# Optimization experiments

Measured on AMD Instinct MI355X. Metric: run time of the kernel, lower is better.

## Reference

```python
import jax, jax.numpy as jnp
import numpy as np

N = 12000
E = 384000
F_IN, F_HID, F_OUT = 512, 256, 64


def setup_inputs() -> dict:
    key = jax.random.key(0)
    ks = jax.random.split(key, 8)
    x = jax.random.normal(ks[0], (N, F_IN), dtype=jnp.float32)
    edge_index = jax.random.randint(ks[1], (2, E), 0, N, dtype=jnp.int64)
    s = lambda fi: 1.0 / np.sqrt(fi)  # glorot-ish scaling
    W1 = jax.random.normal(ks[2], (F_IN, F_HID), dtype=jnp.float32) * s(F_IN)
    W2 = jax.random.normal(ks[3], (F_HID, F_HID), dtype=jnp.float32) * s(F_HID)
    Wmu = jax.random.normal(ks[4], (F_HID, F_OUT), dtype=jnp.float32) * s(F_HID)
    Wls = jax.random.normal(ks[5], (F_HID, F_OUT), dtype=jnp.float32) * s(F_HID)
    return {
        "x": x, "edge_index": edge_index,
        "W1": W1, "b1": jnp.zeros((F_HID,), jnp.float32),
        "W2": W2, "b2": jnp.zeros((F_HID,), jnp.float32),
        "Wmu": Wmu, "bmu": jnp.zeros((F_OUT,), jnp.float32),
        "Wls": Wls, "bls": jnp.zeros((F_OUT,), jnp.float32),
    }


def _gcn_norm(edge_index, n):
    # add self-loops, symmetric normalization D^-1/2 (A+I) D^-1/2 (PyG gcn_norm)
    loop = jnp.arange(n, dtype=edge_index.dtype)
    row = jnp.concatenate([edge_index[0], loop])
    col = jnp.concatenate([edge_index[1], loop])
    deg = jax.ops.segment_sum(jnp.ones(row.shape[0], jnp.float32), col, num_segments=n)
    dinv = jnp.where(deg > 0, jax.lax.rsqrt(jnp.maximum(deg, 1.0)), 0.0)
    norm = dinv[row] * dinv[col]  # [E + n]
    return row, col, norm


def _gcn_conv(h, W, b, row, col, norm, n):
    hw = h @ W                                    # [n, f_out] linear first
    msg = norm[:, None] * hw[row]                 # gather + per-edge scale
    out = jax.ops.segment_sum(msg, col, num_segments=n)  # scatter-add
    return out + b


def reference(x, edge_index, W1, b1, W2, b2, Wmu, bmu, Wls, bls):
    n = x.shape[0]
    row, col, norm = _gcn_norm(edge_index, n)
    h = jax.nn.relu(_gcn_conv(x, W1, b1, row, col, norm, n))
    h = jax.nn.relu(_gcn_conv(h, W2, b2, row, col, norm, n))
    mu = _gcn_conv(h, Wmu, bmu, row, col, norm, n)
    logstd = _gcn_conv(h, Wls, bls, row, col, norm, n)  # computed by encode; unused in eval z
    z = mu  # VGAE.reparametrize in eval mode returns mu (deterministic reference)
    adj_pred = jax.nn.sigmoid(z @ z.T)  # InnerProductDecoder.forward_all
    return adj_pred
```

## Files before the change

kernel.cpp:

```cpp
#include <hip/hip_runtime.h>

#define NN   12000
#define NE   384000
#define FIN  512
#define FHID 256
#define FOUT 64

typedef unsigned short u16;
typedef __attribute__((ext_vector_type(8))) short  s8v;
typedef __attribute__((ext_vector_type(4))) float  f4v;

__device__ __forceinline__ u16 f2bf(float f) {
    union { float f; unsigned int i; } v; v.f = f;
    return (u16)((v.i + 0x7FFFu + ((v.i >> 16) & 1u)) >> 16);
}


__global__ void k_deg(const int* __restrict__ col, float* __restrict__ deg) {
    int e = blockIdx.x * 256 + threadIdx.x;
    if (e < NE) atomicAdd(&deg[col[e]], 1.0f);
}

__global__ __launch_bounds__(1024) void k_scan(const float* __restrict__ deg,
                                               float* __restrict__ dinv,
                                               int* __restrict__ offs,
                                               int* __restrict__ cursor) {
    __shared__ int sh[1024];
    int tid = threadIdx.x;
    int base = tid * 12;
    int loc[12];
    int sum = 0;
    for (int j = 0; j < 12; j++) {
        int i = base + j;
        int d = (i < NN) ? (int)deg[i] : 0;
        loc[j] = sum;
        sum += d;
    }
    sh[tid] = sum;
    __syncthreads();
    for (int off = 1; off < 1024; off <<= 1) {
        int v = (tid >= off) ? sh[tid - off] : 0;
        __syncthreads();
        sh[tid] += v;
        __syncthreads();
    }
    int prev = (tid == 0) ? 0 : sh[tid - 1];
    for (int j = 0; j < 12; j++) {
        int i = base + j;
        if (i < NN) {
            int o = prev + loc[j];
            offs[i] = o;
            cursor[i] = o;
            dinv[i] = rsqrtf(deg[i] + 1.0f);
        }
    }
    if (tid == 0) offs[NN] = NE;
}

__global__ void k_fill(const int* __restrict__ row, const int* __restrict__ col,
                       int* __restrict__ cursor, int* __restrict__ csr) {
    int e = blockIdx.x * 256 + threadIdx.x;
    if (e < NE) {
        int c = col[e];
        int p = atomicAdd(&cursor[c], 1);
        csr[p] = row[e];
    }
}

__global__ void k_repack(const float* __restrict__ B, u16* __restrict__ Bp, int K, int N) {
    int idx = blockIdx.x * 256 + threadIdx.x;
    int total = (N >> 4) * (K >> 5) * 64;
    if (idx >= total) return;
    int l  = idx & 63;
    int ts = idx >> 6;
    int Ks = K >> 5;
    int s  = ts % Ks;
    int t  = ts / Ks;
    int q = l >> 4, r = l & 15;
    s8v v;
    #pragma unroll
    for (int j = 0; j < 8; j++)
        v[j] = (short)f2bf(B[(s * 32 + q * 8 + j) * N + t * 16 + r]);
    ((s8v*)Bp)[idx] = v;
}

template <int K, int N>
__global__ __launch_bounds__(256) void k_gemm(const float* __restrict__ A,
                                              const u16* __restrict__ Bp,
                                              const float* __restrict__ dinv,
                                              float* __restrict__ C) {
    constexpr int KS = K / 32;
    int wave = threadIdx.x >> 6, lane = threadIdx.x & 63;
    int q = lane >> 4, r = lane & 15;
    int row0 = blockIdx.x * 64 + wave * 16;
    if (row0 >= NN) return;
    int tb = blockIdx.y * 4;

    f4v acc[4];
    #pragma unroll
    for (int t = 0; t < 4; t++) acc[t] = (f4v){0.f, 0.f, 0.f, 0.f};

    const float* arow = A + (size_t)(row0 + r) * K + q * 8;
    #pragma unroll 4
    for (int s = 0; s < KS; s++) {
        f4v f0 = *(const f4v*)(arow + s * 32);
        f4v f1 = *(const f4v*)(arow + s * 32 + 4);
        s8v a;
        #pragma unroll
        for (int j = 0; j < 4; j++) { a[j] = (short)f2bf(f0[j]); a[4 + j] = (short)f2bf(f1[j]); }
        #pragma unroll
        for (int t = 0; t < 4; t++) {
            s8v b = *(const s8v*)(Bp + ((((size_t)(tb + t) * KS + s) * 64 + lane) << 3));
            acc[t] = __builtin_amdgcn_mfma_f32_16x16x32_bf16(a, b, acc[t], 0, 0, 0);
        }
    }
    float dv[4];
    #pragma unroll
    for (int rr = 0; rr < 4; rr++) dv[rr] = dinv[row0 + q * 4 + rr];
    #pragma unroll
    for (int t = 0; t < 4; t++) {
        int n = (tb + t) * 16 + r;
        #pragma unroll
        for (int rr = 0; rr < 4; rr++) {
            int m = row0 + q * 4 + rr;
            C[(size_t)m * N + n] = acc[t][rr] * dv[rr];
        }
    }
}

template <int FPL, bool RELU>
__global__ __launch_bounds__(256) void k_agg(const float* __restrict__ hw,
                                             const int* __restrict__ csr,
                                             const int* __restrict__ offs,
                                             const float* __restrict__ dinv,
                                             const float* __restrict__ bias,
                                             float* __restrict__ out) {
    constexpr int F = FPL * 64;
    int wg = (blockIdx.x * 256 + threadIdx.x) >> 6;
    if (wg >= NN) return;
    int lane = threadIdx.x & 63;
    int c = wg;

    float acc[FPL];
    {
        const float* p = hw + (size_t)c * F + lane * FPL;
        if constexpr (FPL == 4) {
            f4v v = *(const f4v*)p;
            #pragma unroll
            for (int k = 0; k < 4; k++) acc[k] = v[k];
        } else {
            acc[0] = *p;
        }
    }
    int beg = offs[c], end = offs[c + 1];
    for (int e = beg; e < end; e += 64) {
        int nb = end - e; if (nb > 64) nb = 64;
        int myid = (e + lane < end) ? csr[e + lane] : 0;
        for (int j = 0; j < nb; j++) {
            int src = __shfl(myid, j, 64);
            const float* p = hw + (size_t)src * F + lane * FPL;
            if constexpr (FPL == 4) {
                f4v v = *(const f4v*)p;
                #pragma unroll
                for (int k = 0; k < 4; k++) acc[k] += v[k];
            } else {
                acc[0] += *p;
            }
        }
    }
    float dv = dinv[c];
    if constexpr (FPL == 4) {
        f4v ov;
        #pragma unroll
        for (int k = 0; k < 4; k++) {
            float val = acc[k] * dv + bias[lane * 4 + k];
            if (RELU) val = fmaxf(val, 0.f);
            ov[k] = val;
        }
        *(f4v*)(out + (size_t)c * F + lane * 4) = ov;
    } else {
        float val = acc[0] * dv + bias[lane];
        if (RELU) val = fmaxf(val, 0.f);
        out[(size_t)c * F + lane] = val;
    }
}

__global__ __launch_bounds__(256) void k_dec(const float* __restrict__ mu, float* __restrict__ out) {
    int wave = threadIdx.x >> 6, lane = threadIdx.x & 63;
    int q = lane >> 4, r = lane & 15;
    int row0 = blockIdx.y * 64 + wave * 16;
    if (row0 >= NN) return;
    int col0 = blockIdx.x * 64;

    s8v a0, a1;
    {
        const float* ap = mu + (size_t)(row0 + r) * FOUT + q * 8;
        f4v f0 = *(const f4v*)(ap);
        f4v f1 = *(const f4v*)(ap + 4);
        f4v f2 = *(const f4v*)(ap + 32);
        f4v f3 = *(const f4v*)(ap + 36);
        #pragma unroll
        for (int j = 0; j < 4; j++) {
            a0[j] = (short)f2bf(f0[j]); a0[4 + j] = (short)f2bf(f1[j]);
            a1[j] = (short)f2bf(f2[j]); a1[4 + j] = (short)f2bf(f3[j]);
        }
    }

    #pragma unroll
    for (int t = 0; t < 4; t++) {
        int n0 = col0 + t * 16;
        if (n0 >= NN) return;
        s8v b0, b1;
        const float* bp = mu + (size_t)(n0 + r) * FOUT + q * 8;
        f4v f0 = *(const f4v*)(bp);
        f4v f1 = *(const f4v*)(bp + 4);
        f4v f2 = *(const f4v*)(bp + 32);
        f4v f3 = *(const f4v*)(bp + 36);
        #pragma unroll
        for (int j = 0; j < 4; j++) {
            b0[j] = (short)f2bf(f0[j]); b0[4 + j] = (short)f2bf(f1[j]);
            b1[j] = (short)f2bf(f2[j]); b1[4 + j] = (short)f2bf(f3[j]);
        }
        f4v acc = (f4v){0.f, 0.f, 0.f, 0.f};
        acc = __builtin_amdgcn_mfma_f32_16x16x32_bf16(a0, b0, acc, 0, 0, 0);
        acc = __builtin_amdgcn_mfma_f32_16x16x32_bf16(a1, b1, acc, 0, 0, 0);
        #pragma unroll
        for (int rr = 0; rr < 4; rr++) {
            int m = row0 + q * 4 + rr;
            float sg = 1.0f / (1.0f + __expf(-acc[rr]));
            out[(size_t)m * NN + (n0 + r)] = sg;
        }
    }
}

extern "C" void kernel_launch(void* const* d_in, const int* in_sizes, int n_in,
                              void* d_out, int out_size, void* d_ws, size_t ws_size,
                              hipStream_t stream) {
    const float* x   = (const float*)d_in[0];
    const int*   ei  = (const int*)d_in[1];
    const float* W1  = (const float*)d_in[2];
    const float* b1  = (const float*)d_in[3];
    const float* W2  = (const float*)d_in[4];
    const float* b2  = (const float*)d_in[5];
    const float* Wmu = (const float*)d_in[6];
    const float* bmu = (const float*)d_in[7];

    char* w = (char*)d_ws;
    size_t off = 0;
    auto alloc = [&](size_t bytes) {
        void* p = w + off;
        off = (off + bytes + 255) & ~(size_t)255;
        return p;
    };
    float* deg    = (float*)alloc(NN * 4);
    float* dinv   = (float*)alloc(NN * 4);
    int*   offs   = (int*)alloc((NN + 1) * 4);
    int*   cursor = (int*)alloc(NN * 4);
    int*   csr    = (int*)alloc(NE * 4);
    float* hw     = (float*)alloc((size_t)NN * FHID * 4);
    float* hA     = (float*)alloc((size_t)NN * FHID * 4);
    float* hB     = (float*)alloc((size_t)NN * FHID * 4);
    float* muB    = (float*)alloc((size_t)NN * FOUT * 4);
    u16*   W1p    = (u16*)alloc((size_t)FIN * FHID * 2);
    u16*   W2p    = (u16*)alloc((size_t)FHID * FHID * 2);
    u16*   Wmp    = (u16*)alloc((size_t)FHID * FOUT * 2);

    const int* erow = ei;
    const int* ecol = ei + NE;

    hipMemsetAsync(deg, 0, NN * 4, stream);
    k_deg<<<(NE + 255) / 256, 256, 0, stream>>>(ecol, deg);
    k_scan<<<1, 1024, 0, stream>>>(deg, dinv, offs, cursor);
    k_fill<<<(NE + 255) / 256, 256, 0, stream>>>(erow, ecol, cursor, csr);

    k_repack<<<((FIN / 32) * (FHID / 16) * 64 + 255) / 256, 256, 0, stream>>>(W1, W1p, FIN, FHID);
    k_repack<<<((FHID / 32) * (FHID / 16) * 64 + 255) / 256, 256, 0, stream>>>(W2, W2p, FHID, FHID);
    k_repack<<<((FHID / 32) * (FOUT / 16) * 64 + 255) / 256, 256, 0, stream>>>(Wmu, Wmp, FHID, FOUT);

    dim3 blk(256);
    k_gemm<FIN, FHID><<<dim3(188, FHID / 64), blk, 0, stream>>>(x, W1p, dinv, hw);
    k_agg<4, true><<<NN / 4, blk, 0, stream>>>(hw, csr, offs, dinv, b1, hA);
    k_gemm<FHID, FHID><<<dim3(188, FHID / 64), blk, 0, stream>>>(hA, W2p, dinv, hw);
    k_agg<4, true><<<NN / 4, blk, 0, stream>>>(hw, csr, offs, dinv, b2, hB);
    k_gemm<FHID, FOUT><<<dim3(188, FOUT / 64), blk, 0, stream>>>(hB, Wmp, dinv, hw);
    k_agg<1, false><<<NN / 4, blk, 0, stream>>>(hw, csr, offs, dinv, bmu, muB);
    k_dec<<<dim3(188, 188), blk, 0, stream>>>(muB, (float*)d_out);
}
```

Baseline: 1.051 ms.

## Vectorize output stores via swapped MFMA operands, bf16 mu, unrolled gathers

Result: faster. 907.4 us (-13.7%).

```diff
diff --git a/kernel.cpp b/kernel.cpp
--- a/kernel.cpp
+++ b/kernel.cpp
@@ -111,125 +111,130 @@
         #pragma unroll
         for (int t = 0; t < 4; t++) {
             s8v b = *(const s8v*)(Bp + ((((size_t)(tb + t) * KS + s) * 64 + lane) << 3));
-            acc[t] = __builtin_amdgcn_mfma_f32_16x16x32_bf16(a, b, acc[t], 0, 0, 0);
-        }
-    }
-    float dv[4];
-    #pragma unroll
-    for (int rr = 0; rr < 4; rr++) dv[rr] = dinv[row0 + q * 4 + rr];
+            acc[t] = __builtin_amdgcn_mfma_f32_16x16x32_bf16(b, a, acc[t], 0, 0, 0);
+        }
+    }
+    float dv = dinv[row0 + r];
+    float* crow = C + (size_t)(row0 + r) * N;
     #pragma unroll
     for (int t = 0; t < 4; t++) {
-        int n = (tb + t) * 16 + r;
-        #pragma unroll
-        for (int rr = 0; rr < 4; rr++) {
-            int m = row0 + q * 4 + rr;
-            C[(size_t)m * N + n] = acc[t][rr] * dv[rr];
-        }
-    }
-}
-
-template <int FPL, bool RELU>
+        f4v ov = acc[t] * dv;
+        *(f4v*)(crow + (tb + t) * 16 + q * 4) = ov;
+    }
+}
+
+template <bool RELU>
 __global__ __launch_bounds__(256) void k_agg(const float* __restrict__ hw,
                                              const int* __restrict__ csr,
                                              const int* __restrict__ offs,
                                              const float* __restrict__ dinv,
                                              const float* __restrict__ bias,
                                              float* __restrict__ out) {
-    constexpr int F = FPL * 64;
+    constexpr int F = 256;
     int wg = (blockIdx.x * 256 + threadIdx.x) >> 6;
     if (wg >= NN) return;
     int lane = threadIdx.x & 63;
     int c = wg;
-
-    float acc[FPL];
-    {
-        const float* p = hw + (size_t)c * F + lane * FPL;
-        if constexpr (FPL == 4) {
-            f4v v = *(const f4v*)p;
-            #pragma unroll
-            for (int k = 0; k < 4; k++) acc[k] = v[k];
-        } else {
-            acc[0] = *p;
-        }
-    }
+    const float* hp = hw + lane * 4;
+
+    f4v acc = *(const f4v*)(hp + (size_t)c * F);
     int beg = offs[c], end = offs[c + 1];
     for (int e = beg; e < end; e += 64) {
         int nb = end - e; if (nb > 64) nb = 64;
         int myid = (e + lane < end) ? csr[e + lane] : 0;
-        for (int j = 0; j < nb; j++) {
-            int src = __shfl(myid, j, 64);
-            const float* p = hw + (size_t)src * F + lane * FPL;
-            if constexpr (FPL == 4) {
-                f4v v = *(const f4v*)p;
-                #pragma unroll
-                for (int k = 0; k < 4; k++) acc[k] += v[k];
-            } else {
-                acc[0] += *p;
-            }
+        int j = 0;
+        for (; j + 4 <= nb; j += 4) {
+            int s0 = __shfl(myid, j, 64);
+            int s1 = __shfl(myid, j + 1, 64);
+            int s2 = __shfl(myid, j + 2, 64);
+            int s3 = __shfl(myid, j + 3, 64);
+            f4v v0 = *(const f4v*)(hp + (size_t)s0 * F);
+            f4v v1 = *(const f4v*)(hp + (size_t)s1 * F);
+            f4v v2 = *(const f4v*)(hp + (size_t)s2 * F);
+            f4v v3 = *(const f4v*)(hp + (size_t)s3 * F);
+            v0 += v1; v2 += v3;
+            acc += v0 + v2;
+        }
+        for (; j < nb; j++) {
+            int s0 = __shfl(myid, j, 64);
+            acc += *(const f4v*)(hp + (size_t)s0 * F);
         }
     }
     float dv = dinv[c];
-    if constexpr (FPL == 4) {
-        f4v ov;
-        #pragma unroll
-        for (int k = 0; k < 4; k++) {
-            float val = acc[k] * dv + bias[lane * 4 + k];
-            if (RELU) val = fmaxf(val, 0.f);
-            ov[k] = val;
-        }
-        *(f4v*)(out + (size_t)c * F + lane * 4) = ov;
-    } else {
-        float val = acc[0] * dv + bias[lane];
-        if (RELU) val = fmaxf(val, 0.f);
-        out[(size_t)c * F + lane] = val;
-    }
-}
-
-__global__ __launch_bounds__(256) void k_dec(const float* __restrict__ mu, float* __restrict__ out) {
+    f4v bv = *(const f4v*)(bias + lane * 4);
+    f4v ov = acc * dv + bv;
+    if (RELU) {
+        #pragma unroll
+        for (int k = 0; k < 4; k++) ov[k] = fmaxf(ov[k], 0.f);
+    }
+    *(f4v*)(out + (size_t)c * F + lane * 4) = ov;
+}
+
+__global__ __launch_bounds__(256) void k_agg_mu(const float* __restrict__ hw,
+                                                const int* __restrict__ csr,
+                                                const int* __restrict__ offs,
+                                                const float* __restrict__ dinv,
+                                                const float* __restrict__ bias,
+                                                u16* __restrict__ out) {
+    constexpr int F = 64;
+    int wg = (blockIdx.x * 256 + threadIdx.x) >> 6;
+    if (wg >= NN) return;
+    int lane = threadIdx.x & 63;
+    int c = wg;
+    const float* hp = hw + lane;
+
+    float acc = hp[(size_t)c * F];
+    int beg = offs[c], end = offs[c + 1];
+    for (int e = beg; e < end; e += 64) {
+        int nb = end - e; if (nb > 64) nb = 64;
+        int myid = (e + lane < end) ? csr[e + lane] : 0;
+        int j = 0;
+        for (; j + 4 <= nb; j += 4) {
+            int s0 = __shfl(myid, j, 64);
+            int s1 = __shfl(myid, j + 1, 64);
+            int s2 = __shfl(myid, j + 2, 64);
+            int s3 = __shfl(myid, j + 3, 64);
+            float v0 = hp[(size_t)s0 * F];
+            float v1 = hp[(size_t)s1 * F];
+            float v2 = hp[(size_t)s2 * F];
+            float v3 = hp[(size_t)s3 * F];
+            acc += (v0 + v1) + (v2 + v3);
+        }
+        for (; j < nb; j++)
+            acc += hp[(size_t)__shfl(myid, j, 64) * F];
+    }
+    out[(size_t)c * F + lane] = f2bf(acc * dinv[c] + bias[lane]);
+}
+
+__global__ __launch_bounds__(256) void k_dec(const u16* __restrict__ mu, float* __restrict__ out) {
     int wave = threadIdx.x >> 6, lane = threadIdx.x & 63;
     int q = lane >> 4, r = lane & 15;
     int row0 = blockIdx.y * 64 + wave * 16;
     if (row0 >= NN) return;
     int col0 = blockIdx.x * 64;
 
-    s8v a0, a1;
-    {
-        const float* ap = mu + (size_t)(row0 + r) * FOUT + q * 8;
-        f4v f0 = *(const f4v*)(ap);
-        f4v f1 = *(const f4v*)(ap + 4);
-        f4v f2 = *(const f4v*)(ap + 32);
-        f4v f3 = *(const f4v*)(ap + 36);
-        #pragma unroll
-        for (int j = 0; j < 4; j++) {
-            a0[j] = (short)f2bf(f0[j]); a0[4 + j] = (short)f2bf(f1[j]);
-            a1[j] = (short)f2bf(f2[j]); a1[4 + j] = (short)f2bf(f3[j]);
-        }
-    }
+    const u16* ap = mu + (size_t)(row0 + r) * FOUT + q * 8;
+    s8v a0 = *(const s8v*)(ap);
+    s8v a1 = *(const s8v*)(ap + 32);
+    float* orow = out + (size_t)(row0 + r) * NN;
 
     #pragma unroll
     for (int t = 0; t < 4; t++) {
         int n0 = col0 + t * 16;
         if (n0 >= NN) return;
-        s8v b0, b1;
-        const float* bp = mu + (size_t)(n0 + r) * FOUT + q * 8;
-        f4v f0 = *(const f4v*)(bp);
-        f4v f1 = *(const f4v*)(bp + 4);
-        f4v f2 = *(const f4v*)(bp + 32);
-        f4v f3 = *(const f4v*)(bp + 36);
-        #pragma unroll
-        for (int j = 0; j < 4; j++) {
-            b0[j] = (short)f2bf(f0[j]); b0[4 + j] = (short)f2bf(f1[j]);
-            b1[j] = (short)f2bf(f2[j]); b1[4 + j] = (short)f2bf(f3[j]);
-        }
+        const u16* bp = mu + (size_t)(n0 + r) * FOUT + q * 8;
+        s8v b0 = *(const s8v*)(bp);
+        s8v b1 = *(const s8v*)(bp + 32);
         f4v acc = (f4v){0.f, 0.f, 0.f, 0.f};
-        acc = __builtin_amdgcn_mfma_f32_16x16x32_bf16(a0, b0, acc, 0, 0, 0);
-        acc = __builtin_amdgcn_mfma_f32_16x16x32_bf16(a1, b1, acc, 0, 0, 0);
+        acc = __builtin_amdgcn_mfma_f32_16x16x32_bf16(b0, a0, acc, 0, 0, 0);
+        acc = __builtin_amdgcn_mfma_f32_16x16x32_bf16(b1, a1, acc, 0, 0, 0);
+        f4v ov;
         #pragma unroll
         for (int rr = 0; rr < 4; rr++) {
-            int m = row0 + q * 4 + rr;
-            float sg = 1.0f / (1.0f + __expf(-acc[rr]));
-            out[(size_t)m * NN + (n0 + r)] = sg;
-        }
+            float e = __expf(-acc[rr]);
+            ov[rr] = __builtin_amdgcn_rcpf(1.0f + e);
+        }
+        *(f4v*)(orow + n0 + q * 4) = ov;
     }
 }
 
@@ -260,7 +265,7 @@
     float* hw     = (float*)alloc((size_t)NN * FHID * 4);
     float* hA     = (float*)alloc((size_t)NN * FHID * 4);
     float* hB     = (float*)alloc((size_t)NN * FHID * 4);
-    float* muB    = (float*)alloc((size_t)NN * FOUT * 4);
+    u16*   muB    = (u16*)alloc((size_t)NN * FOUT * 2);
     u16*   W1p    = (u16*)alloc((size_t)FIN * FHID * 2);
     u16*   W2p    = (u16*)alloc((size_t)FHID * FHID * 2);
     u16*   Wmp    = (u16*)alloc((size_t)FHID * FOUT * 2);
@@ -279,10 +284,10 @@
 
     dim3 blk(256);
     k_gemm<FIN, FHID><<<dim3(188, FHID / 64), blk, 0, stream>>>(x, W1p, dinv, hw);
-    k_agg<4, true><<<NN / 4, blk, 0, stream>>>(hw, csr, offs, dinv, b1, hA);
+    k_agg<true><<<NN / 4, blk, 0, stream>>>(hw, csr, offs, dinv, b1, hA);
     k_gemm<FHID, FHID><<<dim3(188, FHID / 64), blk, 0, stream>>>(hA, W2p, dinv, hw);
-    k_agg<4, true><<<NN / 4, blk, 0, stream>>>(hw, csr, offs, dinv, b2, hB);
+    k_agg<true><<<NN / 4, blk, 0, stream>>>(hw, csr, offs, dinv, b2, hB);
     k_gemm<FHID, FOUT><<<dim3(188, FOUT / 64), blk, 0, stream>>>(hB, Wmp, dinv, hw);
-    k_agg<1, false><<<NN / 4, blk, 0, stream>>>(hw, csr, offs, dinv, bmu, muB);
+    k_agg_mu<<<NN / 4, blk, 0, stream>>>(hw, csr, offs, dinv, bmu, muB);
     k_dec<<<dim3(188, 188), blk, 0, stream>>>(muB, (float*)d_out);
 }
```
